# Kernel tuning notes

Measured on AMD Instinct MI355X. Metric: run time of the kernel, lower is better.

The kernel has to match this reference:

```python
import jax, jax.numpy as jnp
import numpy as np

N, D, R = 32768, 64, 32
EPS = 1e-12


def setup_inputs() -> dict:
    key = jax.random.key(0)
    k1, k2, k3, k4 = jax.random.split(key, 4)
    Xz = jax.random.normal(k1, (N, D), dtype=jnp.float32)
    centers = jax.random.normal(k2, (R, D), dtype=jnp.float32)
    # positive rule widths in [0.5, 1.5)
    sigmas = jax.random.uniform(k3, (R, D), dtype=jnp.float32) + 0.5
    theta = jax.random.normal(k4, (R, D + 1), dtype=jnp.float32)
    return {"Xz": Xz, "centers": centers, "sigmas": sigmas, "theta": theta}


def reference(Xz, centers, sigmas, theta):
    n, d = Xz.shape
    r = centers.shape[0]
    # per-rule Gaussian log-membership: (N, R)
    z = (Xz[:, None, :] - centers[None, :, :]) / (sigmas[None, :, :] + EPS)
    log_w = -0.5 * jnp.sum(z * z, axis=-1)
    # softmax-style normalization with the original's epsilon in the denominator
    w = jnp.exp(log_w - jnp.max(log_w, axis=1, keepdims=True))
    w = w / (jnp.sum(w, axis=1, keepdims=True) + EPS)  # (N, R)
    # design matrix: for each rule r, [w_r, w_r * x] -> (N, R*(1+D))
    X1 = jnp.concatenate([jnp.ones((n, 1), dtype=Xz.dtype), Xz], axis=1)  # (N, 1+D)
    Phi = (w[:, :, None] * X1[:, None, :]).reshape(n, r * (d + 1))
    y = Phi @ theta.reshape(-1)  # (N,)
    return y[:, None], w, Phi
```

## Files before the change

kernel.cpp:

```cpp
#include <hip/hip_runtime.h>
#include <string.h>


constexpr int N_ROWS = 32768;
constexpr int D = 64;
constexpr int R = 32;
constexpr float EPS = 1e-12f;
constexpr int ROWS_PER_BLOCK = 8;
constexpr int BLOCK = 256;
constexpr int PHI_COLS = R * (D + 1);

__global__ __launch_bounds__(BLOCK) void tsk_kernel(
    const float* __restrict__ Xz,
    const float* __restrict__ centers,
    const float* __restrict__ sigmas,
    const float* __restrict__ theta,
    float* __restrict__ y_out,
    float* __restrict__ w_out,
    float* __restrict__ phi_out)
{
    __shared__ float c_lds[R][D + 1];
    __shared__ float is_lds[R][D + 1];
    __shared__ float th_lds[R][D + 1];
    __shared__ float x_lds[ROWS_PER_BLOCK][D + 1];
    __shared__ float w_lds[ROWS_PER_BLOCK][R + 1];

    const int tid = threadIdx.x;
    const int row0 = blockIdx.x * ROWS_PER_BLOCK;

    for (int i = tid; i < R * D; i += BLOCK) {
        int r = i >> 6, d = i & 63;
        c_lds[r][d] = centers[i];
        is_lds[r][d] = 1.0f / (sigmas[i] + EPS);
    }
    for (int i = tid; i < R * (D + 1); i += BLOCK)
        th_lds[i / 65][i % 65] = theta[i];

    if (tid < 128) {
        const float4* x4 = (const float4*)(Xz + (size_t)row0 * D);
        float4 v = x4[tid];
        int e = 4 * tid;
        int rr = e >> 6, cc = e & 63;
        x_lds[rr][cc]     = v.x;
        x_lds[rr][cc + 1] = v.y;
        x_lds[rr][cc + 2] = v.z;
        x_lds[rr][cc + 3] = v.w;
    }
    __syncthreads();

    const int lrow = tid >> 5;
    const int r = tid & 31;
    float acc = 0.0f;
    float tdot = th_lds[r][0];
#pragma unroll
    for (int d = 0; d < D; ++d) {
        float x = x_lds[lrow][d];
        float z = (x - c_lds[r][d]) * is_lds[r][d];
        acc = fmaf(z, z, acc);
        tdot = fmaf(th_lds[r][d + 1], x, tdot);
    }
    float logw = -0.5f * acc;

    float m = logw;
#pragma unroll
    for (int off = 16; off >= 1; off >>= 1)
        m = fmaxf(m, __shfl_xor(m, off, 32));
    float ex = __expf(logw - m);
    float s = ex;
#pragma unroll
    for (int off = 16; off >= 1; off >>= 1)
        s += __shfl_xor(s, off, 32);
    float w = ex / (s + EPS);
    w_lds[lrow][r] = w;
    w_out[(size_t)(row0 + lrow) * R + r] = w;

    float yc = w * tdot;
#pragma unroll
    for (int off = 16; off >= 1; off >>= 1)
        yc += __shfl_xor(yc, off, 32);
    if (r == 0) y_out[row0 + lrow] = yc;
    __syncthreads();

    for (int k = tid; k < PHI_COLS / 4; k += BLOCK) {
        int e = 4 * k;
        int r0 = (e + 0) / 65, j0 = (e + 0) - r0 * 65;
        int r1 = (e + 1) / 65, j1 = (e + 1) - r1 * 65;
        int r2 = (e + 2) / 65, j2 = (e + 2) - r2 * 65;
        int r3 = (e + 3) / 65, j3 = (e + 3) - r3 * 65;
#pragma unroll
        for (int row = 0; row < ROWS_PER_BLOCK; ++row) {
            float4 o;
            o.x = w_lds[row][r0] * ((j0 == 0) ? 1.0f : x_lds[row][j0 - 1]);
            o.y = w_lds[row][r1] * ((j1 == 0) ? 1.0f : x_lds[row][j1 - 1]);
            o.z = w_lds[row][r2] * ((j2 == 0) ? 1.0f : x_lds[row][j2 - 1]);
            o.w = w_lds[row][r3] * ((j3 == 0) ? 1.0f : x_lds[row][j3 - 1]);
            ((float4*)(phi_out + (size_t)(row0 + row) * PHI_COLS))[k] = o;
        }
    }
}

extern "C" void kernel_launch(void* const* d_in, const int* in_sizes, int n_in,
                              void* d_out, int out_size, void* d_ws, size_t ws_size,
                              hipStream_t stream) {
    const float* Xz      = (const float*)d_in[0];
    const float* centers = (const float*)d_in[1];
    const float* sigmas  = (const float*)d_in[2];
    const float* theta   = (const float*)d_in[3];

    float* out = (float*)d_out;
    float* y_out   = out;
    float* w_out   = out + N_ROWS;
    float* phi_out = out + N_ROWS + (size_t)N_ROWS * R;

    dim3 grid(N_ROWS / ROWS_PER_BLOCK);
    tsk_kernel<<<grid, BLOCK, 0, stream>>>(Xz, centers, sigmas, theta,
                                           y_out, w_out, phi_out);
}
```

Before: 300.9 us.

## Split fused kernel into weight/output kernel and Phi-writing kernel

Splits the single kernel into two launches. The first computes memberships, normalized weights and y, handling 32 rows per block so each block's parameter staging is amortized over more rows. The second re-reads Xz and the stored weights and writes the large Phi matrix with a lightweight high-occupancy kernel, using a prepended ones column to drop the per-element branch. This removes the heavy LDS footprint and the mid-kernel barrier from the store-bound Phi phase, at the cost of a second launch and rereading w and Xz from memory.

```diff
diff --git a/kernel.cpp b/kernel.cpp
--- a/kernel.cpp
+++ b/kernel.cpp
@@ -1,99 +1,139 @@
 #include <hip/hip_runtime.h>
-#include <string.h>
 
 
 constexpr int N_ROWS = 32768;
 constexpr int D = 64;
 constexpr int R = 32;
 constexpr float EPS = 1e-12f;
-constexpr int ROWS_PER_BLOCK = 8;
-constexpr int BLOCK = 256;
 constexpr int PHI_COLS = R * (D + 1);
 
-__global__ __launch_bounds__(BLOCK) void tsk_kernel(
+constexpr int A_ROWS = 32;
+constexpr int A_BLOCK = 256;
+
+__global__ __launch_bounds__(A_BLOCK) void wy_kernel(
     const float* __restrict__ Xz,
     const float* __restrict__ centers,
     const float* __restrict__ sigmas,
     const float* __restrict__ theta,
     float* __restrict__ y_out,
-    float* __restrict__ w_out,
-    float* __restrict__ phi_out)
+    float* __restrict__ w_out)
 {
     __shared__ float c_lds[R][D + 1];
     __shared__ float is_lds[R][D + 1];
     __shared__ float th_lds[R][D + 1];
-    __shared__ float x_lds[ROWS_PER_BLOCK][D + 1];
-    __shared__ float w_lds[ROWS_PER_BLOCK][R + 1];
+    __shared__ float x_lds[A_ROWS][D + 1];
 
     const int tid = threadIdx.x;
-    const int row0 = blockIdx.x * ROWS_PER_BLOCK;
+    const int row0 = blockIdx.x * A_ROWS;
 
-    for (int i = tid; i < R * D; i += BLOCK) {
+    for (int i = tid; i < R * D; i += A_BLOCK) {
         int r = i >> 6, d = i & 63;
         c_lds[r][d] = centers[i];
         is_lds[r][d] = 1.0f / (sigmas[i] + EPS);
     }
-    for (int i = tid; i < R * (D + 1); i += BLOCK)
+    for (int i = tid; i < R * (D + 1); i += A_BLOCK)
         th_lds[i / 65][i % 65] = theta[i];
+
+    {
+        const float4* x4 = (const float4*)(Xz + (size_t)row0 * D);
+#pragma unroll
+        for (int t = tid; t < A_ROWS * D / 4; t += A_BLOCK) {
+            float4 v = x4[t];
+            int e = 4 * t;
+            int rr = e >> 6, cc = e & 63;
+            x_lds[rr][cc]     = v.x;
+            x_lds[rr][cc + 1] = v.y;
+            x_lds[rr][cc + 2] = v.z;
+            x_lds[rr][cc + 3] = v.w;
+        }
+    }
+    __syncthreads();
+
+    const int r = tid & 31;
+#pragma unroll
+    for (int sub = 0; sub < A_ROWS / 8; ++sub) {
+        const int lrow = sub * 8 + (tid >> 5);
+        float acc = 0.0f;
+        float tdot = th_lds[r][0];
+#pragma unroll
+        for (int d = 0; d < D; ++d) {
+            float x = x_lds[lrow][d];
+            float z = (x - c_lds[r][d]) * is_lds[r][d];
+            acc = fmaf(z, z, acc);
+            tdot = fmaf(th_lds[r][d + 1], x, tdot);
+        }
+        float logw = -0.5f * acc;
+
+        float m = logw;
+#pragma unroll
+        for (int off = 16; off >= 1; off >>= 1)
+            m = fmaxf(m, __shfl_xor(m, off, 32));
+        float ex = __expf(logw - m);
+        float s = ex;
+#pragma unroll
+        for (int off = 16; off >= 1; off >>= 1)
+            s += __shfl_xor(s, off, 32);
+        float w = ex / (s + EPS);
+        w_out[(size_t)(row0 + lrow) * R + r] = w;
+
+        float yc = w * tdot;
+#pragma unroll
+        for (int off = 16; off >= 1; off >>= 1)
+            yc += __shfl_xor(yc, off, 32);
+        if (r == 0) y_out[row0 + lrow] = yc;
+    }
+}
+
+constexpr int B_ROWS = 8;
+constexpr int B_BLOCK = 256;
+
+__global__ __launch_bounds__(B_BLOCK, 8) void phi_kernel(
+    const float* __restrict__ Xz,
+    const float* __restrict__ w_in,
+    float* __restrict__ phi_out)
+{
+    __shared__ float x1_lds[B_ROWS][66];
+    __shared__ float w_lds[B_ROWS][R + 1];
+
+    const int tid = threadIdx.x;
+    const int row0 = blockIdx.x * B_ROWS;
 
     if (tid < 128) {
         const float4* x4 = (const float4*)(Xz + (size_t)row0 * D);
         float4 v = x4[tid];
         int e = 4 * tid;
-        int rr = e >> 6, cc = e & 63;
-        x_lds[rr][cc]     = v.x;
-        x_lds[rr][cc + 1] = v.y;
-        x_lds[rr][cc + 2] = v.z;
-        x_lds[rr][cc + 3] = v.w;
+        int rr = e >> 6, cc = (e & 63) + 1;
+        x1_lds[rr][cc]     = v.x;
+        x1_lds[rr][cc + 1] = v.y;
+        x1_lds[rr][cc + 2] = v.z;
+        x1_lds[rr][cc + 3] = v.w;
     }
+    if (tid < 64) {
+        const float4* w4 = (const float4*)(w_in + (size_t)row0 * R);
+        float4 v = w4[tid];
+        int e = 4 * tid;
+        int rr = e >> 5, cc = e & 31;
+        w_lds[rr][cc]     = v.x;
+        w_lds[rr][cc + 1] = v.y;
+        w_lds[rr][cc + 2] = v.z;
+        w_lds[rr][cc + 3] = v.w;
+    }
+    if (tid < B_ROWS) x1_lds[tid][0] = 1.0f;
     __syncthreads();
 
-    const int lrow = tid >> 5;
-    const int r = tid & 31;
-    float acc = 0.0f;
-    float tdot = th_lds[r][0];
-#pragma unroll
-    for (int d = 0; d < D; ++d) {
-        float x = x_lds[lrow][d];
-        float z = (x - c_lds[r][d]) * is_lds[r][d];
-        acc = fmaf(z, z, acc);
-        tdot = fmaf(th_lds[r][d + 1], x, tdot);
-    }
-    float logw = -0.5f * acc;
-
-    float m = logw;
-#pragma unroll
-    for (int off = 16; off >= 1; off >>= 1)
-        m = fmaxf(m, __shfl_xor(m, off, 32));
-    float ex = __expf(logw - m);
-    float s = ex;
-#pragma unroll
-    for (int off = 16; off >= 1; off >>= 1)
-        s += __shfl_xor(s, off, 32);
-    float w = ex / (s + EPS);
-    w_lds[lrow][r] = w;
-    w_out[(size_t)(row0 + lrow) * R + r] = w;
-
-    float yc = w * tdot;
-#pragma unroll
-    for (int off = 16; off >= 1; off >>= 1)
-        yc += __shfl_xor(yc, off, 32);
-    if (r == 0) y_out[row0 + lrow] = yc;
-    __syncthreads();
-
-    for (int k = tid; k < PHI_COLS / 4; k += BLOCK) {
+    for (int k = tid; k < PHI_COLS / 4; k += B_BLOCK) {
         int e = 4 * k;
         int r0 = (e + 0) / 65, j0 = (e + 0) - r0 * 65;
         int r1 = (e + 1) / 65, j1 = (e + 1) - r1 * 65;
         int r2 = (e + 2) / 65, j2 = (e + 2) - r2 * 65;
         int r3 = (e + 3) / 65, j3 = (e + 3) - r3 * 65;
 #pragma unroll
-        for (int row = 0; row < ROWS_PER_BLOCK; ++row) {
+        for (int row = 0; row < B_ROWS; ++row) {
             float4 o;
-            o.x = w_lds[row][r0] * ((j0 == 0) ? 1.0f : x_lds[row][j0 - 1]);
-            o.y = w_lds[row][r1] * ((j1 == 0) ? 1.0f : x_lds[row][j1 - 1]);
-            o.z = w_lds[row][r2] * ((j2 == 0) ? 1.0f : x_lds[row][j2 - 1]);
-            o.w = w_lds[row][r3] * ((j3 == 0) ? 1.0f : x_lds[row][j3 - 1]);
+            o.x = w_lds[row][r0] * x1_lds[row][j0];
+            o.y = w_lds[row][r1] * x1_lds[row][j1];
+            o.z = w_lds[row][r2] * x1_lds[row][j2];
+            o.w = w_lds[row][r3] * x1_lds[row][j3];
             ((float4*)(phi_out + (size_t)(row0 + row) * PHI_COLS))[k] = o;
         }
     }
@@ -112,7 +152,8 @@
     float* w_out   = out + N_ROWS;
     float* phi_out = out + N_ROWS + (size_t)N_ROWS * R;
 
-    dim3 grid(N_ROWS / ROWS_PER_BLOCK);
-    tsk_kernel<<<grid, BLOCK, 0, stream>>>(Xz, centers, sigmas, theta,
-                                           y_out, w_out, phi_out);
+    wy_kernel<<<dim3(N_ROWS / A_ROWS), A_BLOCK, 0, stream>>>(
+        Xz, centers, sigmas, theta, y_out, w_out);
+    phi_kernel<<<dim3(N_ROWS / B_ROWS), B_BLOCK, 0, stream>>>(
+        Xz, w_out, phi_out);
 }
```

After: 321.2 us. 1.07x slower.
